# Optimization experiments

Measured on AMD Instinct MI355X. Metric: run time of the kernel, lower is better.

## Reference

```python
import jax, jax.numpy as jnp
import numpy as np
from itertools import combinations

NUM_ENT = 7
DIM_ENT = 256
REL_HIDDEN = 256
HIDDEN = 1024
BATCH = 16384
PAIRS = np.array(list(combinations(range(NUM_ENT), 2)), dtype=np.int32)  # [21, 2]


def setup_inputs() -> dict:
    key = jax.random.key(0)
    k1, k2, k3 = jax.random.split(key, 3)
    ctx = jax.random.normal(k1, (BATCH, NUM_ENT * DIM_ENT), dtype=jnp.float32)
    # torch init: uniform(-init_range, init_range) weights, zero bias
    W_rel = jax.random.uniform(k2, (2 * DIM_ENT, REL_HIDDEN), dtype=jnp.float32, minval=-0.01, maxval=0.01)
    b_rel = jnp.zeros((REL_HIDDEN,), dtype=jnp.float32)
    W_fc = jax.random.uniform(k3, (NUM_ENT * DIM_ENT + REL_HIDDEN, HIDDEN), dtype=jnp.float32, minval=-0.01, maxval=0.01)
    b_fc = jnp.zeros((HIDDEN,), dtype=jnp.float32)
    return {"ctx": ctx, "W_rel": W_rel, "b_rel": b_rel, "W_fc": W_fc, "b_fc": b_fc}


def reference(ctx, W_rel, b_rel, W_fc, b_fc):
    B = ctx.shape[0]
    ents = ctx.reshape(B, NUM_ENT, DIM_ENT)
    idx_i = jnp.asarray(PAIRS[:, 0])
    idx_j = jnp.asarray(PAIRS[:, 1])
    # gather both endpoints of each of the 21 pairs: [B, 21, 2*DIM_ENT]
    pair_feat = jnp.concatenate([ents[:, idx_i, :], ents[:, idx_j, :]], axis=-1)
    # batched small Linear + Tanh: [B, 21, REL_HIDDEN]
    rel = jnp.tanh(jnp.einsum("bpe,eh->bph", pair_feat, W_rel) + b_rel)
    # faithful replication of torch: cat pair-major then view(B, rel_hidden, -1).sum(2)
    rel = rel.reshape(B, 21 * REL_HIDDEN).reshape(B, REL_HIDDEN, 21).sum(axis=2)
    inpt = jnp.concatenate([ctx, rel], axis=1)  # [B, input_size]
    # dropout output is discarded in the original forward (no-op); fc1 uses inpt
    out = jnp.tanh(inpt @ W_fc + b_fc)
    return out[None, :, :]  # [1, B, HIDDEN]
```

## Files before the change

kernel.cpp:

```cpp
#include <hip/hip_runtime.h>

typedef unsigned short u16;
typedef unsigned int u32;
typedef __attribute__((ext_vector_type(8))) short short8;
typedef __attribute__((ext_vector_type(4))) float f32x4;
typedef const __attribute__((address_space(1))) unsigned int g_u32;
typedef __attribute__((address_space(3))) unsigned int l_u32;

#define BATCH 16384
#define XCOLS 2048

__device__ __forceinline__ void gload16(const void* g, void* l) {
  __builtin_amdgcn_global_load_lds((g_u32*)g, (l_u32*)l, 16, 0, 0);
}
__device__ __forceinline__ u16 f2bf(float f) {
  u32 x = __builtin_bit_cast(u32, f);
  x += 0x7fffu + ((x >> 16) & 1u);
  return (u16)(x >> 16);
}
__device__ __forceinline__ int swz(int P) { return P ^ (((P >> 7) & 7) << 4); }

__device__ __forceinline__ float fast_tanh(float x) {
  float e = __builtin_amdgcn_exp2f(x * 2.885390081777927f);
  return __builtin_fmaf(-2.0f, __builtin_amdgcn_rcpf(e + 1.0f), 1.0f);
}

#define PIPK 0544333222211111000000ULL
#define PJPK 0665654654365432654321ULL

__global__ void prep_ctx(const float* __restrict__ ctx, u16* __restrict__ X) {
  const int total = BATCH * 224;
  for (int u = blockIdx.x * blockDim.x + threadIdx.x; u < total;
       u += gridDim.x * blockDim.x) {
    int b = u / 224, c8 = u - b * 224;
    const float4* s = (const float4*)(ctx + (size_t)b * 1792 + c8 * 8);
    float4 v0 = s[0], v1 = s[1];
    short8 o;
    o[0] = (short)f2bf(v0.x); o[1] = (short)f2bf(v0.y);
    o[2] = (short)f2bf(v0.z); o[3] = (short)f2bf(v0.w);
    o[4] = (short)f2bf(v1.x); o[5] = (short)f2bf(v1.y);
    o[6] = (short)f2bf(v1.z); o[7] = (short)f2bf(v1.w);
    *(short8*)(X + (size_t)b * XCOLS + c8 * 8) = o;
  }
}

__global__ void prep_wrel(const float* __restrict__ Wr, u16* __restrict__ WcT) {
  int idx = blockIdx.x * 256 + threadIdx.x;
  if (idx >= 512 * 256) return;
  int n = idx >> 8, k = idx & 255;
  float v = (n < 256) ? Wr[k * 256 + n] : Wr[(256 + k) * 256 + (n - 256)];
  WcT[idx] = f2bf(v);
}

__global__ void prep_wfc(const float* __restrict__ W, u16* __restrict__ WT) {
  __shared__ float t[64][65];
  int k0 = blockIdx.x * 64;
  int n0 = blockIdx.y * 64;
  int tx = threadIdx.x & 63, ty = threadIdx.x >> 6;
  #pragma unroll
  for (int i = 0; i < 64; i += 4)
    t[ty + i][tx] = W[(size_t)(k0 + ty + i) * 1024 + n0 + tx];
  __syncthreads();
  #pragma unroll
  for (int i = 0; i < 64; i += 4) {
    int n = ty + i;
    WT[(size_t)(n0 + n) * XCOLS + k0 + tx] = f2bf(t[tx][n]);
  }
}

__global__ __launch_bounds__(512, 4) void gemm1_fused(u16* __restrict__ X, const u16* __restrict__ WcT,
                                                      const float* __restrict__ b_rel) {
  __shared__ __align__(16) u16 smem[36864];
  char* sb = (char*)smem;
  const int tid = threadIdx.x;
  const int wid = tid >> 6, lane = tid & 63;
  const int b_base = blockIdx.x * 8;
  f32x4 bias[4] = {};
  if (wid < 4) {
    #pragma unroll
    for (int n = 0; n < 4; ++n)
      bias[n] = *(const f32x4*)(b_rel + wid * 64 + n * 16 + ((lane >> 4) << 2));
  }
  f32x4 acc[4][4] = {};
  for (int kt = 0; kt < 4; ++kt) {
    const int kb = kt * 64;
    {
      int L = swz(tid * 16);
      int row = L >> 7, koff = (L & 127) >> 1;
      int r = row < 56 ? row : 55;
      int bl = r / 7, e = r - bl * 7;
      gload16(X + (size_t)(b_base + bl) * XCOLS + e * 256 + kb + koff, sb + wid * 1024);
    }
    #pragma unroll
    for (int i = 0; i < 8; ++i) {
      int slot = i * 512 + tid;
      int L = swz(slot * 16);
      int rn = L >> 7, koff = (L & 127) >> 1;
      gload16(WcT + rn * 256 + kb + koff, sb + 8192 + (i * 512 + wid * 64) * 16);
    }
    __syncthreads();
    #pragma unroll
    for (int kk = 0; kk < 64; kk += 32) {
      short8 a[4], b[4];
      #pragma unroll
      for (int m = 0; m < 4; ++m) {
        int row = m * 16 + (lane & 15);
        int L = row * 128 + kk * 2 + ((lane >> 4) << 4);
        a[m] = *(const short8*)(sb + swz(L));
      }
      #pragma unroll
      for (int n = 0; n < 4; ++n) {
        int rn = wid * 64 + n * 16 + (lane & 15);
        int L = rn * 128 + kk * 2 + ((lane >> 4) << 4);
        b[n] = *(const short8*)(sb + 8192 + swz(L));
      }
      #pragma unroll
      for (int m = 0; m < 4; ++m)
        #pragma unroll
        for (int n = 0; n < 4; ++n)
          acc[m][n] = __builtin_amdgcn_mfma_f32_16x16x32_bf16(b[n], a[m], acc[m][n], 0, 0, 0);
    }
    __syncthreads();
  }
  float* Tbuf = (float*)(sb + 28672);
  auto stage = [&](int rd) {
    #pragma unroll
    for (int m = 0; m < 4; ++m) {
      int row = m * 16 + (lane & 15);
      int lr = row - rd * 14;
      if (lr >= 0 && lr < 14) {
        #pragma unroll
        for (int n = 0; n < 4; ++n) {
          f32x4 val = acc[m][n] + bias[n];
          int h0 = wid * 64 + n * 16 + ((lane >> 4) << 2);
          int L = lr * 2048 + h0 * 4;
          *(f32x4*)(sb + (L ^ ((lr & 7) << 4))) = val;
        }
      }
    }
  };
  stage(0);
  __syncthreads();
  for (int rd = 0; rd < 4; ++rd) {
    for (int i = tid; i < 2688; i += 512) {
      int bb = i >= 1344;
      int k4 = (i - bb * 1344) << 2;
      int p = k4 >> 8, h0 = k4 & 255;
      int li = bb * 7 + (int)((PIPK >> (3 * p)) & 7);
      int lj = bb * 7 + (int)((PJPK >> (3 * p)) & 7);
      int Lu = (li * 2048 + h0 * 4) ^ ((li & 7) << 4);
      int Lv = (lj * 2048 + 1024 + h0 * 4) ^ ((lj & 7) << 4);
      f32x4 uu = *(const f32x4*)(sb + Lu);
      f32x4 vv = *(const f32x4*)(sb + Lv);
      f32x4 t;
      t[0] = fast_tanh(uu[0] + vv[0]);
      t[1] = fast_tanh(uu[1] + vv[1]);
      t[2] = fast_tanh(uu[2] + vv[2]);
      t[3] = fast_tanh(uu[3] + vv[3]);
      *(f32x4*)(sb + 28672 + (bb * 5376 + k4) * 4) = t;
    }
    __syncthreads();
    {
      int bb = tid >> 8, r = tid & 255;
      const float* T = Tbuf + bb * 5376 + r * 21;
      float s = 0.f;
      #pragma unroll
      for (int c = 0; c < 21; ++c) s += T[c];
      X[(size_t)(b_base + rd * 2 + bb) * XCOLS + 1792 + r] = f2bf(s);
    }
    if (rd < 3) stage(rd + 1);
    __syncthreads();
  }
}

#define G2_BUF 49152
__global__ __launch_bounds__(512, 2) void gemm2(const u16* __restrict__ X, const u16* __restrict__ WT,
                                                const float* __restrict__ b_fc, float* __restrict__ out) {
  __shared__ __align__(16) u16 smem[73728];
  char* sb = (char*)smem;
  const int tid = threadIdx.x;
  const int wid = tid >> 6, lane = tid & 63;
  const int wr = wid >> 2, wc = wid & 3;
  int bid = blockIdx.x;
  int sw = (bid & 7) * 64 + (bid >> 3);
  int bm = sw >> 3, bn = sw & 7;
  const size_t mBase = (size_t)bm * 256;
  const int nBase = bn * 128;
  f32x4 acc[8][2] = {};
  auto stage2 = [&](int t, int q) {
    char* Ab = sb + q * G2_BUF;
    char* Bb = Ab + 32768;
    const int kb = t * 64;
    #pragma unroll
    for (int i = 0; i < 4; ++i) {
      int L = swz((i * 512 + tid) * 16);
      int row = L >> 7, koff = (L & 127) >> 1;
      gload16(X + (mBase + row) * XCOLS + kb + koff, Ab + (i * 512 + wid * 64) * 16);
    }
    #pragma unroll
    for (int i = 0; i < 2; ++i) {
      int L = swz((i * 512 + tid) * 16);
      int row = L >> 7, koff = (L & 127) >> 1;
      gload16(WT + (size_t)(nBase + row) * XCOLS + kb + koff, Bb + (i * 512 + wid * 64) * 16);
    }
  };
  auto compute = [&](int q) {
    char* Ab = sb + q * G2_BUF;
    char* Bb = Ab + 32768;
    #pragma unroll
    for (int kk = 0; kk < 64; kk += 32) {
      short8 a[8], b[2];
      #pragma unroll
      for (int m = 0; m < 8; ++m) {
        int row = wr * 128 + m * 16 + (lane & 15);
        int L = row * 128 + kk * 2 + ((lane >> 4) << 4);
        a[m] = *(const short8*)(Ab + swz(L));
      }
      #pragma unroll
      for (int n = 0; n < 2; ++n) {
        int rn = wc * 32 + n * 16 + (lane & 15);
        int L = rn * 128 + kk * 2 + ((lane >> 4) << 4);
        b[n] = *(const short8*)(Bb + swz(L));
      }
      __builtin_amdgcn_s_setprio(1);
      #pragma unroll
      for (int m = 0; m < 8; ++m)
        #pragma unroll
        for (int n = 0; n < 2; ++n)
          acc[m][n] = __builtin_amdgcn_mfma_f32_16x16x32_bf16(a[m], b[n], acc[m][n], 0, 0, 0);
      __builtin_amdgcn_s_setprio(0);
    }
  };
  stage2(0, 0);
  stage2(1, 1);
  int qc = 0;
  for (int t = 0; t < 31; ++t) {
    asm volatile("s_waitcnt vmcnt(6)" ::: "memory");
    __builtin_amdgcn_s_barrier();
    if (t < 30) {
      int qs = qc + 2 >= 3 ? qc - 1 : qc + 2;
      stage2(t + 2, qs);
    }
    compute(qc);
    qc = qc + 1 >= 3 ? 0 : qc + 1;
  }
  asm volatile("s_waitcnt vmcnt(0)" ::: "memory");
  __builtin_amdgcn_s_barrier();
  compute(qc);
  #pragma unroll
  for (int m = 0; m < 8; ++m) {
    int row0 = wr * 128 + m * 16 + ((lane >> 4) << 2);
    #pragma unroll
    for (int n = 0; n < 2; ++n) {
      int col = nBase + wc * 32 + n * 16 + (lane & 15);
      float bias = b_fc[col];
      #pragma unroll
      for (int v = 0; v < 4; ++v)
        out[(mBase + row0 + v) * 1024 + col] = fast_tanh(acc[m][n][v] + bias);
    }
  }
}

extern "C" void kernel_launch(void* const* d_in, const int* in_sizes, int n_in,
                              void* d_out, int out_size, void* d_ws, size_t ws_size,
                              hipStream_t stream) {
  const float* ctx   = (const float*)d_in[0];
  const float* W_rel = (const float*)d_in[1];
  const float* b_rel = (const float*)d_in[2];
  const float* W_fc  = (const float*)d_in[3];
  const float* b_fc  = (const float*)d_in[4];
  float* out = (float*)d_out;
  u16* X    = (u16*)d_ws;
  u16* WcT  = X + (size_t)BATCH * XCOLS;
  u16* WfcT = WcT + 512 * 256;
  prep_ctx<<<2048, 256, 0, stream>>>(ctx, X);
  prep_wrel<<<512, 256, 0, stream>>>(W_rel, WcT);
  prep_wfc<<<dim3(32, 16), 256, 0, stream>>>(W_fc, WfcT);
  gemm1_fused<<<2048, 512, 0, stream>>>(X, WcT, b_rel);
  gemm2<<<512, 512, 0, stream>>>(X, WfcT, b_fc, out);
}
```

Baseline: 193.9 us.

## Enlarge gemm2 tile to 256x256 with double buffering and merge prep kernels

The three preprocessing kernels are merged into one launch that branches on block index, which removes two kernel launches. gemm2 now uses 256x256 output tiles (256 blocks instead of 512), giving each wave 8x4 MFMA accumulators and more arithmetic per byte loaded. The LDS pipeline drops from three stages to two, with an extra barrier before each refill. In exchange, the grid is only 256 blocks, which may underfill the GPU's CUs. Register pressure also doubles the accumulator count, and the prefetch pipeline is shallower.

Measured after the change: 192.3 us, median of 2. Within noise of the previous version (-0.8%).

```diff
diff --git a/kernel.cpp b/kernel.cpp
--- a/kernel.cpp
+++ b/kernel.cpp
@@ -28,43 +28,42 @@
 #define PIPK 0544333222211111000000ULL
 #define PJPK 0665654654365432654321ULL
 
-__global__ void prep_ctx(const float* __restrict__ ctx, u16* __restrict__ X) {
-  const int total = BATCH * 224;
-  for (int u = blockIdx.x * blockDim.x + threadIdx.x; u < total;
-       u += gridDim.x * blockDim.x) {
-    int b = u / 224, c8 = u - b * 224;
-    const float4* s = (const float4*)(ctx + (size_t)b * 1792 + c8 * 8);
-    float4 v0 = s[0], v1 = s[1];
-    short8 o;
-    o[0] = (short)f2bf(v0.x); o[1] = (short)f2bf(v0.y);
-    o[2] = (short)f2bf(v0.z); o[3] = (short)f2bf(v0.w);
-    o[4] = (short)f2bf(v1.x); o[5] = (short)f2bf(v1.y);
-    o[6] = (short)f2bf(v1.z); o[7] = (short)f2bf(v1.w);
-    *(short8*)(X + (size_t)b * XCOLS + c8 * 8) = o;
-  }
-}
-
-__global__ void prep_wrel(const float* __restrict__ Wr, u16* __restrict__ WcT) {
-  int idx = blockIdx.x * 256 + threadIdx.x;
-  if (idx >= 512 * 256) return;
-  int n = idx >> 8, k = idx & 255;
-  float v = (n < 256) ? Wr[k * 256 + n] : Wr[(256 + k) * 256 + (n - 256)];
-  WcT[idx] = f2bf(v);
-}
-
-__global__ void prep_wfc(const float* __restrict__ W, u16* __restrict__ WT) {
+__global__ void prep_all(const float* __restrict__ ctx, const float* __restrict__ Wr,
+                         const float* __restrict__ Wfc, u16* __restrict__ X,
+                         u16* __restrict__ WcT, u16* __restrict__ WfcT) {
   __shared__ float t[64][65];
-  int k0 = blockIdx.x * 64;
-  int n0 = blockIdx.y * 64;
-  int tx = threadIdx.x & 63, ty = threadIdx.x >> 6;
-  #pragma unroll
-  for (int i = 0; i < 64; i += 4)
-    t[ty + i][tx] = W[(size_t)(k0 + ty + i) * 1024 + n0 + tx];
-  __syncthreads();
-  #pragma unroll
-  for (int i = 0; i < 64; i += 4) {
-    int n = ty + i;
-    WT[(size_t)(n0 + n) * XCOLS + k0 + tx] = f2bf(t[tx][n]);
+  const int bid = blockIdx.x, tid = threadIdx.x;
+  if (bid < 2048) {
+    const int total = BATCH * 224;
+    for (int u = bid * 256 + tid; u < total; u += 2048 * 256) {
+      int b = u / 224, c8 = u - b * 224;
+      const float4* s = (const float4*)(ctx + (size_t)b * 1792 + c8 * 8);
+      float4 v0 = s[0], v1 = s[1];
+      short8 o;
+      o[0] = (short)f2bf(v0.x); o[1] = (short)f2bf(v0.y);
+      o[2] = (short)f2bf(v0.z); o[3] = (short)f2bf(v0.w);
+      o[4] = (short)f2bf(v1.x); o[5] = (short)f2bf(v1.y);
+      o[6] = (short)f2bf(v1.z); o[7] = (short)f2bf(v1.w);
+      *(short8*)(X + (size_t)b * XCOLS + c8 * 8) = o;
+    }
+  } else if (bid < 2560) {
+    int b2 = bid - 2048;
+    int k0 = (b2 >> 4) * 64, n0 = (b2 & 15) * 64;
+    int tx = tid & 63, ty = tid >> 6;
+    #pragma unroll
+    for (int i = 0; i < 64; i += 4)
+      t[ty + i][tx] = Wfc[(size_t)(k0 + ty + i) * 1024 + n0 + tx];
+    __syncthreads();
+    #pragma unroll
+    for (int i = 0; i < 64; i += 4) {
+      int n = ty + i;
+      WfcT[(size_t)(n0 + n) * XCOLS + k0 + tx] = f2bf(t[tx][n]);
+    }
+  } else {
+    int idx = (bid - 2560) * 256 + tid;
+    int n = idx >> 8, k = idx & 255;
+    float v = (n < 256) ? Wr[k * 256 + n] : Wr[(256 + k) * 256 + (n - 256)];
+    WcT[idx] = f2bf(v);
   }
 }
 
@@ -173,43 +172,37 @@
   }
 }
 
-#define G2_BUF 49152
+#define G2B 65536
 __global__ __launch_bounds__(512, 2) void gemm2(const u16* __restrict__ X, const u16* __restrict__ WT,
                                                 const float* __restrict__ b_fc, float* __restrict__ out) {
-  __shared__ __align__(16) u16 smem[73728];
+  __shared__ __align__(16) u16 smem[65536];
   char* sb = (char*)smem;
   const int tid = threadIdx.x;
   const int wid = tid >> 6, lane = tid & 63;
   const int wr = wid >> 2, wc = wid & 3;
-  int bid = blockIdx.x;
-  int sw = (bid & 7) * 64 + (bid >> 3);
-  int bm = sw >> 3, bn = sw & 7;
+  const int bm = blockIdx.x >> 2, bn = blockIdx.x & 3;
   const size_t mBase = (size_t)bm * 256;
-  const int nBase = bn * 128;
-  f32x4 acc[8][2] = {};
+  const int nBase = bn * 256;
+  f32x4 acc[8][4] = {};
   auto stage2 = [&](int t, int q) {
-    char* Ab = sb + q * G2_BUF;
+    char* Ab = sb + q * G2B;
     char* Bb = Ab + 32768;
     const int kb = t * 64;
     #pragma unroll
     for (int i = 0; i < 4; ++i) {
       int L = swz((i * 512 + tid) * 16);
       int row = L >> 7, koff = (L & 127) >> 1;
-      gload16(X + (mBase + row) * XCOLS + kb + koff, Ab + (i * 512 + wid * 64) * 16);
-    }
-    #pragma unroll
-    for (int i = 0; i < 2; ++i) {
-      int L = swz((i * 512 + tid) * 16);
-      int row = L >> 7, koff = (L & 127) >> 1;
-      gload16(WT + (size_t)(nBase + row) * XCOLS + kb + koff, Bb + (i * 512 + wid * 64) * 16);
+      int dst = (i * 512 + wid * 64) * 16;
+      gload16(X + (mBase + row) * XCOLS + kb + koff, Ab + dst);
+      gload16(WT + (size_t)(nBase + row) * XCOLS + kb + koff, Bb + dst);
     }
   };
   auto compute = [&](int q) {
-    char* Ab = sb + q * G2_BUF;
+    char* Ab = sb + q * G2B;
     char* Bb = Ab + 32768;
     #pragma unroll
     for (int kk = 0; kk < 64; kk += 32) {
-      short8 a[8], b[2];
+      short8 a[8], b[4];
       #pragma unroll
       for (int m = 0; m < 8; ++m) {
         int row = wr * 128 + m * 16 + (lane & 15);
@@ -217,8 +210,8 @@
         a[m] = *(const short8*)(Ab + swz(L));
       }
       #pragma unroll
-      for (int n = 0; n < 2; ++n) {
-        int rn = wc * 32 + n * 16 + (lane & 15);
+      for (int n = 0; n < 4; ++n) {
+        int rn = wc * 64 + n * 16 + (lane & 15);
         int L = rn * 128 + kk * 2 + ((lane >> 4) << 4);
         b[n] = *(const short8*)(Bb + swz(L));
       }
@@ -226,33 +219,29 @@
       #pragma unroll
       for (int m = 0; m < 8; ++m)
         #pragma unroll
-        for (int n = 0; n < 2; ++n)
+        for (int n = 0; n < 4; ++n)
           acc[m][n] = __builtin_amdgcn_mfma_f32_16x16x32_bf16(a[m], b[n], acc[m][n], 0, 0, 0);
       __builtin_amdgcn_s_setprio(0);
     }
   };
   stage2(0, 0);
   stage2(1, 1);
-  int qc = 0;
-  for (int t = 0; t < 31; ++t) {
-    asm volatile("s_waitcnt vmcnt(6)" ::: "memory");
+  for (int t = 0; t < 32; ++t) {
+    if (t < 30) asm volatile("s_waitcnt vmcnt(8)" ::: "memory");
+    else        asm volatile("s_waitcnt vmcnt(0)" ::: "memory");
     __builtin_amdgcn_s_barrier();
+    compute(t & 1);
     if (t < 30) {
-      int qs = qc + 2 >= 3 ? qc - 1 : qc + 2;
-      stage2(t + 2, qs);
-    }
-    compute(qc);
-    qc = qc + 1 >= 3 ? 0 : qc + 1;
-  }
-  asm volatile("s_waitcnt vmcnt(0)" ::: "memory");
-  __builtin_amdgcn_s_barrier();
-  compute(qc);
+      __builtin_amdgcn_s_barrier();
+      stage2(t + 2, t & 1);
+    }
+  }
   #pragma unroll
   for (int m = 0; m < 8; ++m) {
     int row0 = wr * 128 + m * 16 + ((lane >> 4) << 2);
     #pragma unroll
-    for (int n = 0; n < 2; ++n) {
-      int col = nBase + wc * 32 + n * 16 + (lane & 15);
+    for (int n = 0; n < 4; ++n) {
+      int col = nBase + wc * 64 + n * 16 + (lane & 15);
       float bias = b_fc[col];
       #pragma unroll
       for (int v = 0; v < 4; ++v)
@@ -273,9 +262,7 @@
   u16* X    = (u16*)d_ws;
   u16* WcT  = X + (size_t)BATCH * XCOLS;
   u16* WfcT = WcT + 512 * 256;
-  prep_ctx<<<2048, 256, 0, stream>>>(ctx, X);
-  prep_wrel<<<512, 256, 0, stream>>>(W_rel, WcT);
-  prep_wfc<<<dim3(32, 16), 256, 0, stream>>>(W_fc, WfcT);
+  prep_all<<<3072, 256, 0, stream>>>(ctx, W_rel, W_fc, X, WcT, WfcT);
   gemm1_fused<<<2048, 512, 0, stream>>>(X, WcT, b_rel);
-  gemm2<<<512, 512, 0, stream>>>(X, WfcT, b_fc, out);
-}
+  gemm2<<<256, 512, 0, stream>>>(X, WfcT, b_fc, out);
+}
```
